# Optimization experiments

Measured on AMD Instinct MI355X. Metric: run time of the kernel, lower is better.

Reference implementation:

```python
import jax, jax.numpy as jnp
import numpy as np

N_EMBD = 1024
N_HEAD = 16
HEAD_DIM = N_EMBD // N_HEAD


def setup_inputs() -> dict:
    key = jax.random.key(0)
    kx, kq, kk, kv, ko = jax.random.split(key, 5)
    s = 1.0 / np.sqrt(N_EMBD)
    return {
        "x": jax.random.normal(kx, (4, 2048, N_EMBD), dtype=jnp.float32),
        "Wq": jax.random.normal(kq, (N_EMBD, N_EMBD), dtype=jnp.float32) * s,
        "Wk": jax.random.normal(kk, (N_EMBD, N_EMBD), dtype=jnp.float32) * s,
        "Wv": jax.random.normal(kv, (N_EMBD, N_EMBD), dtype=jnp.float32) * s,
        "Wo": jax.random.normal(ko, (N_EMBD, N_EMBD), dtype=jnp.float32) * s,
    }


def reference(x, Wq, Wk, Wv, Wo):
    B, T, C = x.shape
    H, D = N_HEAD, HEAD_DIM
    # projections; torch Linear computes x @ W.T
    q = (x @ Wq.T).reshape(B, T, H, D).transpose(0, 2, 1, 3)  # [B,H,T,D]
    k = (x @ Wk.T).reshape(B, T, H, D).transpose(0, 2, 1, 3)
    v = (x @ Wv.T).reshape(B, T, H, D).transpose(0, 2, 1, 3)
    scores = jnp.einsum("bhtd,bhsd->bhts", q, k) / np.sqrt(D).astype(np.float32)
    causal = jnp.tril(jnp.ones((T, T), dtype=bool))
    scores = jnp.where(causal, scores, -jnp.inf)
    attn = jax.nn.softmax(scores, axis=-1)
    out = jnp.einsum("bhts,bhsd->bhtd", attn, v)  # [B,H,T,D]
    out = out.transpose(0, 2, 1, 3).reshape(B, T, C)
    return out @ Wo.T
```

## Files before the change

kernel.cpp:

```cpp
#include <hip/hip_runtime.h>
#include <hip/hip_bf16.h>


typedef __bf16 bf16_t;
typedef __bf16 bf16x4 __attribute__((ext_vector_type(4)));
typedef __bf16 bf16x8 __attribute__((ext_vector_type(8)));
typedef float  f32x4  __attribute__((ext_vector_type(4)));

#define MFMA16(a, b, c) __builtin_amdgcn_mfma_f32_16x16x32_bf16(a, b, c, 0, 0, 0)

__device__ __forceinline__ float exp2_(float x) {
#if __has_builtin(__builtin_amdgcn_exp2f)
    return __builtin_amdgcn_exp2f(x);
#else
    return __expf(x * 0.6931471805599453f);
#endif
}

__device__ __forceinline__ void gload_lds16(const bf16_t* g, bf16_t* l) {
    __builtin_amdgcn_global_load_lds(
        (const __attribute__((address_space(1))) void*)g,
        (__attribute__((address_space(3))) void*)l, 16, 0, 0);
}

__global__ __launch_bounds__(256)
void cast_f32_bf16(const float* __restrict__ in, bf16_t* __restrict__ out, int n8) {
    int i = blockIdx.x * 256 + threadIdx.x;
    if (i >= n8) return;
    const float4* p = (const float4*)in;
    float4 a = p[i * 2], b = p[i * 2 + 1];
    bf16x8 o;
    o[0] = (bf16_t)a.x; o[1] = (bf16_t)a.y; o[2] = (bf16_t)a.z; o[3] = (bf16_t)a.w;
    o[4] = (bf16_t)b.x; o[5] = (bf16_t)b.y; o[6] = (bf16_t)b.z; o[7] = (bf16_t)b.w;
    *(bf16x8*)(out + (size_t)i * 8) = o;
}

__global__ __launch_bounds__(256)
void cast4_f32_bf16(const float* __restrict__ i0, const float* __restrict__ i1,
                    const float* __restrict__ i2, const float* __restrict__ i3,
                    bf16_t* o0, bf16_t* o1, bf16_t* o2, bf16_t* o3, int n8) {
    const float* in = blockIdx.y == 0 ? i0 : blockIdx.y == 1 ? i1 : blockIdx.y == 2 ? i2 : i3;
    bf16_t*     out = blockIdx.y == 0 ? o0 : blockIdx.y == 1 ? o1 : blockIdx.y == 2 ? o2 : o3;
    int i = blockIdx.x * 256 + threadIdx.x;
    if (i >= n8) return;
    const float4* p = (const float4*)in;
    float4 a = p[i * 2], b = p[i * 2 + 1];
    bf16x8 o;
    o[0] = (bf16_t)a.x; o[1] = (bf16_t)a.y; o[2] = (bf16_t)a.z; o[3] = (bf16_t)a.w;
    o[4] = (bf16_t)b.x; o[5] = (bf16_t)b.y; o[6] = (bf16_t)b.z; o[7] = (bf16_t)b.w;
    *(bf16x8*)(out + (size_t)i * 8) = o;
}

template<int OUT_BF16>
__global__ __launch_bounds__(256)
void gemm_bt(const bf16_t* __restrict__ A, const bf16_t* __restrict__ B,
             void* __restrict__ Cv, int M, int N, int K) {
    __shared__ bf16_t As[128 * 32];
    __shared__ bf16_t Bs[128 * 32];
    const int tid = threadIdx.x;
    const int lane = tid & 63;
    const int w = tid >> 6;
    const int wm = w >> 1, wn = w & 1;
    const int g = lane >> 4, c = lane & 15;
    const long bm = (long)blockIdx.x * 128;
    const long bn = (long)blockIdx.y * 128;

    f32x4 acc[4][4] = {};

    const int srow = tid >> 2;
    const int scol = (tid & 3) << 3;
    const bf16_t* Ag = A + (bm + srow) * (long)K + scol;
    const bf16_t* Bg = B + (bn + srow) * (long)K + scol;
    bf16_t* AsW = As + tid * 8;
    bf16_t* BsW = Bs + tid * 8;

    for (int k0 = 0; k0 < K; k0 += 32) {
        gload_lds16(Ag + k0,                 AsW);
        gload_lds16(Ag + k0 + (long)64 * K,  AsW + 2048);
        gload_lds16(Bg + k0,                 BsW);
        gload_lds16(Bg + k0 + (long)64 * K,  BsW + 2048);
        __syncthreads();
        bf16x8 af[4], bfr[4];
        #pragma unroll
        for (int m = 0; m < 4; ++m)
            af[m] = *(const bf16x8*)(As + (wm * 64 + m * 16 + c) * 32 + g * 8);
        #pragma unroll
        for (int n = 0; n < 4; ++n)
            bfr[n] = *(const bf16x8*)(Bs + (wn * 64 + n * 16 + c) * 32 + g * 8);
        #pragma unroll
        for (int m = 0; m < 4; ++m)
            #pragma unroll
            for (int n = 0; n < 4; ++n)
                acc[m][n] = MFMA16(af[m], bfr[n], acc[m][n]);
        __syncthreads();
    }
    #pragma unroll
    for (int m = 0; m < 4; ++m)
        #pragma unroll
        for (int n = 0; n < 4; ++n)
            #pragma unroll
            for (int i = 0; i < 4; ++i) {
                long row = bm + wm * 64 + m * 16 + g * 4 + i;
                long col = bn + wn * 64 + n * 16 + c;
                float v = acc[m][n][i];
                if (OUT_BF16) ((bf16_t*)Cv)[row * N + col] = (bf16_t)v;
                else          ((float*)Cv)[row * N + col]  = v;
            }
}


__device__ __forceinline__ void stage_K(const bf16_t* Kp, long rowb, int kb, int hcol,
                                        bf16_t* Kbuf, int tid) {
    int row = tid >> 3;
    int lb  = (tid & 7) ^ (row & 7);
    gload_lds16(Kp + (rowb + kb + row) * 3072 + hcol + lb * 8, Kbuf + tid * 8);
}

__device__ __forceinline__ bf16x8 load_V8(const bf16_t* Vp, long rowb, int kb,
                                          int hcol, int tid) {
    const int d  = tid & 63;
    const int k0 = (tid >> 6) * 8;
    bf16x8 v;
    #pragma unroll
    for (int j = 0; j < 8; ++j)
        v[j] = Vp[(rowb + kb + k0 + j) * 3072 + hcol + d];
    return v;
}

__device__ __forceinline__ void write_V8(bf16_t* Vbuf, int tid, bf16x8 v) {
    const int d  = tid & 63;
    const int k0 = (tid >> 6) * 8;
    *(bf16x8*)&Vbuf[d * 72 + k0] = v;
}

__global__ __launch_bounds__(512, 6)
void attn_kernel(const bf16_t* __restrict__ Qp, const bf16_t* __restrict__ Kp,
                 const bf16_t* __restrict__ Vp, bf16_t* __restrict__ O) {
    __shared__ bf16_t Ks[2][64 * 64];
    __shared__ bf16_t Vts[2][64 * 72];
    __shared__ bf16_t PW[8][16 * 72];

    const int tid = threadIdx.x, lane = tid & 63, w = tid >> 6;
    const int g = lane >> 4, c = lane & 15;
    const int bh = blockIdx.x;
    const int b = bh >> 4, h = bh & 15;
    const long rowb = (long)b * 2048;
    const int hcol = h * 64;
    const float QSCL = 0.18033688011112042f;

    const int q0  = 15 - blockIdx.y;
    const int qlo = q0 * 128 + w * 16;
    const int nkt = 2 * q0 + 2;

    bf16x8 qf[2];
    #pragma unroll
    for (int ks = 0; ks < 2; ++ks) {
        qf[ks] = *(const bf16x8*)(Qp + (rowb + qlo + c) * 3072 +
                                  hcol + ks * 32 + g * 8);
        #pragma unroll
        for (int j = 0; j < 8; ++j)
            qf[ks][j] = (bf16_t)((float)qf[ks][j] * QSCL);
    }

    float m_r = -1e30f, l_r = 0.f;
    f32x4 acc[4] = {};

    stage_K(Kp, rowb, 0, hcol, Ks[0], tid);
    write_V8(Vts[0], tid, load_V8(Vp, rowb, 0, hcol, tid));
    __syncthreads();

    for (int t = 0; t < nkt; ++t) {
        const int cur = t & 1;
        const int kb = t * 64;
        const bool pre = (t + 1 < nkt);
        bf16x8 vreg;
        if (pre) {
            stage_K(Kp, rowb, kb + 64, hcol, Ks[cur ^ 1], tid);
            vreg = load_V8(Vp, rowb, kb + 64, hcol, tid);
        }

        if (kb <= qlo + 15) {
            f32x4 sacc[4] = {};
            __builtin_amdgcn_s_setprio(1);
            #pragma unroll
            for (int nt = 0; nt < 4; ++nt) {
                const int row = nt * 16 + c;
                #pragma unroll
                for (int ks = 0; ks < 2; ++ks) {
                    bf16x8 kf = *(const bf16x8*)&Ks[cur][row * 64 +
                                    (((ks * 4 + g) ^ (c & 7)) * 8)];
                    sacc[nt] = MFMA16(kf, qf[ks], sacc[nt]);
                }
            }
            __builtin_amdgcn_s_setprio(0);
            if (kb + 63 > qlo) {
                const int q = qlo + c;
                #pragma unroll
                for (int nt = 0; nt < 4; ++nt)
                    #pragma unroll
                    for (int i = 0; i < 4; ++i) {
                        int key = kb + nt * 16 + g * 4 + i;
                        if (key > q) sacc[nt][i] = -1e30f;
                    }
            }

            float mx01a = fmaxf(sacc[0][0], sacc[0][1]);
            float mx01b = fmaxf(sacc[0][2], sacc[0][3]);
            float mx11a = fmaxf(sacc[1][0], sacc[1][1]);
            float mx11b = fmaxf(sacc[1][2], sacc[1][3]);
            float mx21a = fmaxf(sacc[2][0], sacc[2][1]);
            float mx21b = fmaxf(sacc[2][2], sacc[2][3]);
            float mx31a = fmaxf(sacc[3][0], sacc[3][1]);
            float mx31b = fmaxf(sacc[3][2], sacc[3][3]);
            float mx = fmaxf(fmaxf(fmaxf(mx01a, mx01b), fmaxf(mx11a, mx11b)),
                             fmaxf(fmaxf(mx21a, mx21b), fmaxf(mx31a, mx31b)));
            mx = fmaxf(mx, __shfl_xor(mx, 16, 64));
            mx = fmaxf(mx, __shfl_xor(mx, 32, 64));
            if (__any(mx > m_r + 8.f)) {
                float mnew = fmaxf(m_r, mx);
                float scl = exp2_(m_r - mnew);
                #pragma unroll
                for (int nt = 0; nt < 4; ++nt)
                    acc[nt] *= scl;
                l_r *= scl;
                m_r = mnew;
            }
            float rsn[4];
            #pragma unroll
            for (int nt = 0; nt < 4; ++nt) {
                #pragma unroll
                for (int i = 0; i < 4; ++i)
                    sacc[nt][i] = exp2_(sacc[nt][i] - m_r);
                rsn[nt] = (sacc[nt][0] + sacc[nt][1]) + (sacc[nt][2] + sacc[nt][3]);
            }
            float rs = (rsn[0] + rsn[1]) + (rsn[2] + rsn[3]);
            rs += __shfl_xor(rs, 16, 64);
            rs += __shfl_xor(rs, 32, 64);
            l_r += rs;

            #pragma unroll
            for (int nt = 0; nt < 4; ++nt) {
                bf16x4 t4;
                #pragma unroll
                for (int i = 0; i < 4; ++i) t4[i] = (bf16_t)sacc[nt][i];
                *(bf16x4*)&PW[w][c * 72 + nt * 16 + g * 4] = t4;
            }

            __builtin_amdgcn_s_setprio(1);
            #pragma unroll
            for (int ks = 0; ks < 2; ++ks) {
                bf16x8 pf = *(const bf16x8*)&PW[w][c * 72 + ks * 32 + g * 8];
                #pragma unroll
                for (int nt = 0; nt < 4; ++nt) {
                    bf16x8 vf = *(const bf16x8*)&Vts[cur][(nt * 16 + c) * 72 +
                                                          ks * 32 + g * 8];
                    acc[nt] = MFMA16(vf, pf, acc[nt]);
                }
            }
            __builtin_amdgcn_s_setprio(0);
        }

        if (pre) write_V8(Vts[cur ^ 1], tid, vreg);
        __syncthreads();
    }

    {
        float rl = __builtin_amdgcn_rcpf(l_r);
        #pragma unroll
        for (int nt = 0; nt < 4; ++nt) {
            bf16x4 t4;
            #pragma unroll
            for (int i = 0; i < 4; ++i) t4[i] = (bf16_t)(acc[nt][i] * rl);
            *(bf16x4*)&PW[w][c * 72 + nt * 16 + g * 4] = t4;
        }
    }
    #pragma unroll
    for (int p = 0; p < 2; ++p) {
        int row = p * 8 + (lane >> 3);
        int ch  = (lane & 7) * 8;
        bf16x8 v = *(const bf16x8*)&PW[w][row * 72 + ch];
        *(bf16x8*)&O[(rowb + qlo + row) * 1024 + hcol + ch] = v;
    }
}

extern "C" void kernel_launch(void* const* d_in, const int* in_sizes, int n_in,
                              void* d_out, int out_size, void* d_ws, size_t ws_size,
                              hipStream_t stream) {
    const float* x  = (const float*)d_in[0];
    const float* Wq = (const float*)d_in[1];
    const float* Wk = (const float*)d_in[2];
    const float* Wv = (const float*)d_in[3];
    const float* Wo = (const float*)d_in[4];

    const int M = 8192;
    const int C = 1024;

    char* ws = (char*)d_ws;
    bf16_t* xb   = (bf16_t*)(ws);
    bf16_t* wqkv = (bf16_t*)(ws + ((size_t)16 << 20));
    bf16_t* wob  = (bf16_t*)(ws + ((size_t)22 << 20));
    bf16_t* qkv  = (bf16_t*)(ws + ((size_t)24 << 20));
    bf16_t* aob  = (bf16_t*)(ws + ((size_t)72 << 20));

    cast_f32_bf16<<<(M * C / 8) / 256, 256, 0, stream>>>(x, xb, M * C / 8);
    cast4_f32_bf16<<<dim3((C * C / 8) / 256, 4), 256, 0, stream>>>(
        Wq, Wk, Wv, Wo,
        wqkv, wqkv + (size_t)(C * C), wqkv + (size_t)(2 * C * C), wob, C * C / 8);

    gemm_bt<1><<<dim3(M / 128, 3072 / 128), 256, 0, stream>>>(xb, wqkv, qkv, M, 3072, C);

    attn_kernel<<<dim3(64, 16), 512, 0, stream>>>(
        qkv, qkv + 1024, qkv + 2048, aob);

    gemm_bt<0><<<dim3(M / 128, C / 128), 256, 0, stream>>>(aob, wob, d_out, M, C, C);
}
```

Measured before the change: 188.1 us.

## Merge cast kernels and defer softmax row reductions in attention

The separate cast kernels for x and for the four weights are merged into one launch with a 2D grid. The second grid row maps each thread to one of Wq/Wk/Wv/Wo by index. In the attention loop, the cross-lane max shuffle now runs only inside the rare rescale branch. The row-sum shuffle reduction moves out of the loop and runs once before normalisation. This cuts one kernel launch and several cross-lane shuffles per key tile, in exchange for slightly more index logic in the cast kernel.

```diff
diff --git a/kernel.cpp b/kernel.cpp
--- a/kernel.cpp
+++ b/kernel.cpp
@@ -24,31 +24,30 @@
 }
 
 __global__ __launch_bounds__(256)
-void cast_f32_bf16(const float* __restrict__ in, bf16_t* __restrict__ out, int n8) {
+void cast_all(const float* __restrict__ x,  const float* __restrict__ Wq,
+              const float* __restrict__ Wk, const float* __restrict__ Wv,
+              const float* __restrict__ Wo,
+              bf16_t* __restrict__ xb, bf16_t* __restrict__ wqkv,
+              bf16_t* __restrict__ wob) {
     int i = blockIdx.x * 256 + threadIdx.x;
-    if (i >= n8) return;
-    const float4* p = (const float4*)in;
+    const float* src;
+    bf16_t* dst;
+    if (blockIdx.y == 0) {
+        src = x; dst = xb;
+    } else {
+        if (i >= 524288) return;
+        int wsel = i >> 17;
+        int loc  = i & 131071;
+        src = wsel == 0 ? Wq : wsel == 1 ? Wk : wsel == 2 ? Wv : Wo;
+        dst = wsel == 3 ? wob : wqkv + (size_t)wsel * 1048576;
+        i = loc;
+    }
+    const float4* p = (const float4*)src;
     float4 a = p[i * 2], b = p[i * 2 + 1];
     bf16x8 o;
     o[0] = (bf16_t)a.x; o[1] = (bf16_t)a.y; o[2] = (bf16_t)a.z; o[3] = (bf16_t)a.w;
     o[4] = (bf16_t)b.x; o[5] = (bf16_t)b.y; o[6] = (bf16_t)b.z; o[7] = (bf16_t)b.w;
-    *(bf16x8*)(out + (size_t)i * 8) = o;
-}
-
-__global__ __launch_bounds__(256)
-void cast4_f32_bf16(const float* __restrict__ i0, const float* __restrict__ i1,
-                    const float* __restrict__ i2, const float* __restrict__ i3,
-                    bf16_t* o0, bf16_t* o1, bf16_t* o2, bf16_t* o3, int n8) {
-    const float* in = blockIdx.y == 0 ? i0 : blockIdx.y == 1 ? i1 : blockIdx.y == 2 ? i2 : i3;
-    bf16_t*     out = blockIdx.y == 0 ? o0 : blockIdx.y == 1 ? o1 : blockIdx.y == 2 ? o2 : o3;
-    int i = blockIdx.x * 256 + threadIdx.x;
-    if (i >= n8) return;
-    const float4* p = (const float4*)in;
-    float4 a = p[i * 2], b = p[i * 2 + 1];
-    bf16x8 o;
-    o[0] = (bf16_t)a.x; o[1] = (bf16_t)a.y; o[2] = (bf16_t)a.z; o[3] = (bf16_t)a.w;
-    o[4] = (bf16_t)b.x; o[5] = (bf16_t)b.y; o[6] = (bf16_t)b.z; o[7] = (bf16_t)b.w;
-    *(bf16x8*)(out + (size_t)i * 8) = o;
+    *(bf16x8*)(dst + (size_t)i * 8) = o;
 }
 
 template<int OUT_BF16>
@@ -162,7 +161,8 @@
             qf[ks][j] = (bf16_t)((float)qf[ks][j] * QSCL);
     }
 
-    float m_r = -1e30f, l_r = 0.f;
+    float m_r = -1e30f;
+    float l_r = 0.f;
     f32x4 acc[4] = {};
 
     stage_K(Kp, rowb, 0, hcol, Ks[0], tid);
@@ -204,19 +204,17 @@
                     }
             }
 
-            float mx01a = fmaxf(sacc[0][0], sacc[0][1]);
-            float mx01b = fmaxf(sacc[0][2], sacc[0][3]);
-            float mx11a = fmaxf(sacc[1][0], sacc[1][1]);
-            float mx11b = fmaxf(sacc[1][2], sacc[1][3]);
-            float mx21a = fmaxf(sacc[2][0], sacc[2][1]);
-            float mx21b = fmaxf(sacc[2][2], sacc[2][3]);
-            float mx31a = fmaxf(sacc[3][0], sacc[3][1]);
-            float mx31b = fmaxf(sacc[3][2], sacc[3][3]);
-            float mx = fmaxf(fmaxf(fmaxf(mx01a, mx01b), fmaxf(mx11a, mx11b)),
-                             fmaxf(fmaxf(mx21a, mx21b), fmaxf(mx31a, mx31b)));
-            mx = fmaxf(mx, __shfl_xor(mx, 16, 64));
-            mx = fmaxf(mx, __shfl_xor(mx, 32, 64));
+            float m0 = fmaxf(fmaxf(sacc[0][0], sacc[0][1]),
+                             fmaxf(fmaxf(sacc[0][2], sacc[0][3]), sacc[1][0]));
+            float m1 = fmaxf(fmaxf(sacc[1][1], sacc[1][2]),
+                             fmaxf(fmaxf(sacc[1][3], sacc[2][0]), sacc[2][1]));
+            float m2 = fmaxf(fmaxf(sacc[2][2], sacc[2][3]),
+                             fmaxf(fmaxf(sacc[3][0], sacc[3][1]),
+                                   fmaxf(sacc[3][2], sacc[3][3])));
+            float mx = fmaxf(fmaxf(m0, m1), m2);
             if (__any(mx > m_r + 8.f)) {
+                mx = fmaxf(mx, __shfl_xor(mx, 16, 64));
+                mx = fmaxf(mx, __shfl_xor(mx, 32, 64));
                 float mnew = fmaxf(m_r, mx);
                 float scl = exp2_(m_r - mnew);
                 #pragma unroll
@@ -233,10 +231,7 @@
                     sacc[nt][i] = exp2_(sacc[nt][i] - m_r);
                 rsn[nt] = (sacc[nt][0] + sacc[nt][1]) + (sacc[nt][2] + sacc[nt][3]);
             }
-            float rs = (rsn[0] + rsn[1]) + (rsn[2] + rsn[3]);
-            rs += __shfl_xor(rs, 16, 64);
-            rs += __shfl_xor(rs, 32, 64);
-            l_r += rs;
+            l_r += (rsn[0] + rsn[1]) + (rsn[2] + rsn[3]);
 
             #pragma unroll
             for (int nt = 0; nt < 4; ++nt) {
@@ -264,6 +259,8 @@
         __syncthreads();
     }
 
+    l_r += __shfl_xor(l_r, 16, 64);
+    l_r += __shfl_xor(l_r, 32, 64);
     {
         float rl = __builtin_amdgcn_rcpf(l_r);
         #pragma unroll
@@ -302,10 +299,7 @@
     bf16_t* qkv  = (bf16_t*)(ws + ((size_t)24 << 20));
     bf16_t* aob  = (bf16_t*)(ws + ((size_t)72 << 20));
 
-    cast_f32_bf16<<<(M * C / 8) / 256, 256, 0, stream>>>(x, xb, M * C / 8);
-    cast4_f32_bf16<<<dim3((C * C / 8) / 256, 4), 256, 0, stream>>>(
-        Wq, Wk, Wv, Wo,
-        wqkv, wqkv + (size_t)(C * C), wqkv + (size_t)(2 * C * C), wob, C * C / 8);
+    cast_all<<<dim3(4096, 2), 256, 0, stream>>>(x, Wq, Wk, Wv, Wo, xb, wqkv, wob);
 
     gemm_bt<1><<<dim3(M / 128, 3072 / 128), 256, 0, stream>>>(xb, wqkv, qkv, M, 3072, C);
 
```

New measurement: 179.7 us. 1.05x faster.
